# Optimization experiments

Measured on AMD Instinct MI355X. Metric: run time of the kernel, lower is better.

## Reference

```python
import jax, jax.numpy as jnp
import numpy as np

N_SRNA = 20000
N_MRNA = 100000
HID = 128
E_S2M = 1_000_000
E_M2M = 2_000_000
E_LBL = 500_000
N_LAYERS = 2


def setup_inputs() -> dict:
    key = jax.random.key(0)
    ks = jax.random.split(key, 20)
    s = 0.05
    inp = {
        # edge lists (rev edge types are flips, derived inside reference)
        "s2m_src": jax.random.randint(ks[0], (E_S2M,), 0, N_SRNA),
        "s2m_dst": jax.random.randint(ks[1], (E_S2M,), 0, N_MRNA),
        "m2m_src": jax.random.randint(ks[2], (E_M2M,), 0, N_MRNA),
        "m2m_dst": jax.random.randint(ks[3], (E_M2M,), 0, N_MRNA),
        "label_src": jax.random.randint(ks[4], (E_LBL,), 0, N_SRNA),
        "label_dst": jax.random.randint(ks[5], (E_LBL,), 0, N_MRNA),
        # embeddings (node_id is arange over all nodes -> identity lookup)
        "srna_emb": jax.random.normal(ks[6], (N_SRNA, HID), jnp.float32),
        "mrna_emb": jax.random.normal(ks[7], (N_MRNA, HID), jnp.float32),
        # per-layer stacked params. SAGEConv: out = lin_l(mean_agg)+lin_r(x_dst)
        "sage_s2m_Wl": jax.random.normal(ks[8], (N_LAYERS, HID, HID), jnp.float32) * s,
        "sage_s2m_bl": jnp.zeros((N_LAYERS, HID), jnp.float32),
        "sage_s2m_Wr": jax.random.normal(ks[9], (N_LAYERS, HID, HID), jnp.float32) * s,
        "sage_rev_Wl": jax.random.normal(ks[10], (N_LAYERS, HID, HID), jnp.float32) * s,
        "sage_rev_bl": jnp.zeros((N_LAYERS, HID), jnp.float32),
        "sage_rev_Wr": jax.random.normal(ks[11], (N_LAYERS, HID, HID), jnp.float32) * s,
        # GCNConv: out = propagate(norm, x @ W) + b
        "gcn_m2m_W": jax.random.normal(ks[12], (N_LAYERS, HID, HID), jnp.float32) * s,
        "gcn_m2m_b": jnp.zeros((N_LAYERS, HID), jnp.float32),
        "gcn_rev_W": jax.random.normal(ks[13], (N_LAYERS, HID, HID), jnp.float32) * s,
        "gcn_rev_b": jnp.zeros((N_LAYERS, HID), jnp.float32),
    }
    return inp


def _sage(x_src, x_dst, src, dst, n_dst, Wl, bl, Wr):
    # PyG SAGEConv (aggr='mean', root_weight=True): lin_l(mean_msg) + lin_r(x_dst)
    agg = jax.ops.segment_sum(x_src[src], dst, num_segments=n_dst)  # [n_dst, h]
    cnt = jax.ops.segment_sum(jnp.ones((src.shape[0],), x_src.dtype), dst,
                              num_segments=n_dst)
    agg = agg / jnp.maximum(cnt, 1.0)[:, None]
    return agg @ Wl + bl + x_dst @ Wr


def _gcn(x, src, dst, n, W, b):
    # PyG GCNConv: add self-loops, sym-normalize, x @ W, propagate, + bias
    xw = x @ W  # [n, h]
    deg = jax.ops.segment_sum(jnp.ones((src.shape[0],), x.dtype), dst,
                              num_segments=n) + 1.0  # +1 self-loop
    dinv = jax.lax.rsqrt(deg)
    norm = dinv[src] * dinv[dst]  # [E]
    out = jax.ops.segment_sum(norm[:, None] * xw[src], dst, num_segments=n)
    out = out + (dinv * dinv)[:, None] * xw  # self-loop term
    return out + b


def reference(s2m_src, s2m_dst, m2m_src, m2m_dst, label_src, label_dst,
              srna_emb, mrna_emb,
              sage_s2m_Wl, sage_s2m_bl, sage_s2m_Wr,
              sage_rev_Wl, sage_rev_bl, sage_rev_Wr,
              gcn_m2m_W, gcn_m2m_b, gcn_rev_W, gcn_rev_b):
    x_s, x_m = srna_emb, mrna_emb
    for l in range(N_LAYERS):
        # HeteroConv aggr='sum' over edge types per dst node type
        m_new = _sage(x_s, x_m, s2m_src, s2m_dst, N_MRNA,
                      sage_s2m_Wl[l], sage_s2m_bl[l], sage_s2m_Wr[l])
        m_new = m_new + _gcn(x_m, m2m_src, m2m_dst, N_MRNA,
                             gcn_m2m_W[l], gcn_m2m_b[l])
        m_new = m_new + _gcn(x_m, m2m_dst, m2m_src, N_MRNA,
                             gcn_rev_W[l], gcn_rev_b[l])  # rev_similar = flip
        s_new = _sage(x_m, x_s, s2m_dst, s2m_src, N_SRNA,
                      sage_rev_Wl[l], sage_rev_bl[l], sage_rev_Wr[l])
        x_s, x_m = jax.nn.relu(s_new), jax.nn.relu(m_new)
    # Classifier: dot product over labeled (srna, mrna) pairs
    return (x_s[label_src] * x_m[label_dst]).sum(axis=-1)
```

## Files before the change

### kernel.cpp

```cpp
#include <hip/hip_runtime.h>
#include <hip/hip_fp16.h>

#define NS 20000
#define NM 100000
#define H  128
#define ES 1000000
#define EM 2000000
#define EL 500000

#define SH_M 7
#define SH_S 6
#define NB_SD 782
#define NB_SS 313
#define NB_MD 782
#define NB_MS 782
#define CAP_SD 1664
#define CAP_SS 3904
#define CAP_MD 3200
#define CAP_MS 3200
#define MAXCAP 3904
#define CHUNK 4096
#define B_SD ((ES + CHUNK - 1) / CHUNK)
#define B_SS ((ES + CHUNK - 1) / CHUNK)
#define B_MD ((EM + CHUNK - 1) / CHUNK)
#define B_MS ((EM + CHUNK - 1) / CHUNK)
#define VAL_MASK 0x1FFFF

typedef _Float16 half8 __attribute__((ext_vector_type(8)));
typedef float floatx4 __attribute__((ext_vector_type(4)));

__global__ __launch_bounds__(256) void place1_sorted(
        const int* __restrict__ s2m_src, const int* __restrict__ s2m_dst,
        const int* __restrict__ m2m_src, const int* __restrict__ m2m_dst,
        int* __restrict__ bc,
        unsigned int* __restrict__ p_sd, unsigned int* __restrict__ p_ss,
        unsigned int* __restrict__ p_md, unsigned int* __restrict__ p_ms) {
    __shared__ unsigned int rec[CHUNK];
    __shared__ unsigned short eb[CHUNK];
    __shared__ int cnt[1024];
    __shared__ int gbase[1024];

    int b = blockIdx.x;
    const int *keys, *vals; int shift, cap, E, bcoff; unsigned int* pp;
    int cb;
    if (b < B_SD)                    { cb = b;                      keys = s2m_dst; vals = s2m_src; shift = SH_M; cap = CAP_SD; E = ES; bcoff = 0;     pp = p_sd; }
    else if (b < B_SD+B_SS)          { cb = b - B_SD;               keys = s2m_src; vals = s2m_dst; shift = SH_S; cap = CAP_SS; E = ES; bcoff = 16384; pp = p_ss; }
    else if (b < B_SD+B_SS+B_MD)     { cb = b - B_SD - B_SS;        keys = m2m_dst; vals = m2m_src; shift = SH_M; cap = CAP_MD; E = EM; bcoff = 32768; pp = p_md; }
    else                             { cb = b - B_SD - B_SS - B_MD; keys = m2m_src; vals = m2m_dst; shift = SH_M; cap = CAP_MS; E = EM; bcoff = 49152; pp = p_ms; }
    int* bcp = bc + bcoff;

    int t = threadIdx.x;
    int e0 = cb * CHUNK;
    int nv = E - e0; if (nv > CHUNK) nv = CHUNK;

    for (int i = t; i < nv; i += 256) {
        int k = keys[e0 + i];
        int v = vals[e0 + i];
        int bkt = k >> shift;
        rec[i] = ((unsigned int)(k - (bkt << shift)) << 17) | (unsigned int)v;
        eb[i] = (unsigned short)bkt;
    }
#pragma unroll
    for (int j = 0; j < 4; ++j) cnt[t * 4 + j] = 0;
    __syncthreads();
    for (int i = t; i < nv; i += 256) atomicAdd(&cnt[eb[i]], 1);
    __syncthreads();
#pragma unroll
    for (int j = 0; j < 4; ++j) {
        int bk = t * 4 + j;
        int c = cnt[bk];
        if (c > 0) {
            gbase[bk] = atomicAdd(&bcp[bk << 4], c);
            cnt[bk] = 0;
        }
    }
    __syncthreads();
    for (int i = t; i < nv; i += 256) {
        int bk = eb[i];
        int pos = atomicAdd(&cnt[bk], 1);
        int o = gbase[bk] + pos;
        if (o < cap) pp[(size_t)bk * cap + o] = rec[i];
    }
}

__global__ __launch_bounds__(1024) void bscan(const int* __restrict__ bc,
                                              int* __restrict__ bbase) {
    __shared__ int sh[1024];
    int c = blockIdx.x;
    int n = (c == 0) ? NB_SD : (c == 1) ? NB_SS : (c == 2) ? NB_MD : NB_MS;
    const int* bcp = bc + c * 16384;
    int t = threadIdx.x;
    int v = (t < n) ? bcp[t << 4] : 0;
    sh[t] = v;
    __syncthreads();
    for (int d = 1; d < 1024; d <<= 1) {
        int x = 0;
        if (t >= d) x = sh[t - d];
        __syncthreads();
        if (t >= d) sh[t] += x;
        __syncthreads();
    }
    if (t < n) bbase[c * 1024 + t] = sh[t] - v;
}

__global__ __launch_bounds__(256) void place2_fused(
        const int* __restrict__ bc, const int* __restrict__ bbase,
        const unsigned int* __restrict__ p_sd, const unsigned int* __restrict__ p_ss,
        const unsigned int* __restrict__ p_md, const unsigned int* __restrict__ p_ms,
        int* __restrict__ adj_sd, int* __restrict__ adj_ss,
        int* __restrict__ adj_md, int* __restrict__ adj_ms,
        int* __restrict__ off_sd, int* __restrict__ off_ss,
        int* __restrict__ off_md, int* __restrict__ off_ms,
        int* __restrict__ cnt_sd, int* __restrict__ cnt_ss,
        int* __restrict__ cnt_md, int* __restrict__ cnt_ms) {
    __shared__ unsigned int lp[MAXCAP];
    __shared__ int hist[128], cur[128], sbuf[128];
    int b = blockIdx.x;
    int c, lb;
    if (b < NB_SD)                    { c = 0; lb = b; }
    else if (b < NB_SD+NB_SS)         { c = 1; lb = b - NB_SD; }
    else if (b < NB_SD+NB_SS+NB_MD)   { c = 2; lb = b - NB_SD - NB_SS; }
    else                              { c = 3; lb = b - NB_SD - NB_SS - NB_MD; }
    const unsigned int* pp; int *adj, *offp, *cntp; int shift, cap, n;
    switch (c) {
    case 0:  pp = p_sd; adj = adj_sd; offp = off_sd; cntp = cnt_sd; shift = SH_M; cap = CAP_SD; n = NM; break;
    case 1:  pp = p_ss; adj = adj_ss; offp = off_ss; cntp = cnt_ss; shift = SH_S; cap = CAP_SS; n = NS; break;
    case 2:  pp = p_md; adj = adj_md; offp = off_md; cntp = cnt_md; shift = SH_M; cap = CAP_MD; n = NM; break;
    default: pp = p_ms; adj = adj_ms; offp = off_ms; cntp = cnt_ms; shift = SH_M; cap = CAP_MS; n = NM; break;
    }
    int t = threadIdx.x;
    int k = bc[c * 16384 + (lb << 4)];
    if (k > cap) k = cap;
    int base = lb << shift;
    int npb = 1 << shift;
    int bb = bbase[c * 1024 + lb];
    for (int i = t; i < k; i += 256) lp[i] = pp[(size_t)lb * cap + i];
    if (t < npb) hist[t] = 0;
    __syncthreads();
    for (int i = t; i < k; i += 256) atomicAdd(&hist[lp[i] >> 17], 1);
    __syncthreads();
    int v = (t < npb) ? hist[t] : 0;
    if (t < 128) sbuf[t] = v;
    __syncthreads();
    for (int d = 1; d < 128; d <<= 1) {
        int x = 0;
        if (t >= d && t < 128) x = sbuf[t - d];
        __syncthreads();
        if (t >= d && t < 128) sbuf[t] += x;
        __syncthreads();
    }
    if (t < npb) {
        int excl = sbuf[t] - v;
        cur[t] = excl;
        int node = base + t;
        if (node < n) { offp[node] = bb + excl; cntp[node] = v; }
    }
    __syncthreads();
    for (int i = t; i < k; i += 256) {
        unsigned int p = lp[i];
        int pos = atomicAdd(&cur[p >> 17], 1);
        adj[bb + pos] = (int)(p & VAL_MASK);
    }
}

__global__ void finalize_scales(const int* __restrict__ c_md, const int* __restrict__ c_ms,
                                float* __restrict__ dvf, float* __restrict__ dvr) {
    int i = blockIdx.x * blockDim.x + threadIdx.x;
    if (i < NM) {
        dvf[i] = rsqrtf((float)c_md[i] + 1.0f);
        dvr[i] = rsqrtf((float)c_ms[i] + 1.0f);
    }
}

__global__ void to_half(const float* __restrict__ in, __half* __restrict__ out,
                        long long n4) {
    long long i = (long long)blockIdx.x * blockDim.x + threadIdx.x;
    if (i >= n4) return;
    float4 v = *(const float4*)&in[i * 4];
    __half2 h0 = __floats2half2_rn(v.x, v.y);
    __half2 h1 = __floats2half2_rn(v.z, v.w);
    __half2* o = (__half2*)&out[i * 4];
    o[0] = h0; o[1] = h1;
}

__global__ void prep_w(const float* __restrict__ w0, const float* __restrict__ w1,
                       const float* __restrict__ w2, const float* __restrict__ w3,
                       const float* __restrict__ w4, const float* __restrict__ w5,
                       __half* __restrict__ out) {
    int idx = blockIdx.x * 256 + threadIdx.x;
    if (idx >= 12 * H * H) return;
    int mat = idx / (H * H);
    int rem = idx % (H * H);
    int n = rem / H;
    int k = rem % H;
    const float* base;
    switch (mat >> 1) {
    case 0: base = w0; break; case 1: base = w1; break; case 2: base = w2; break;
    case 3: base = w3; break; case 4: base = w4; break; default: base = w5; break;
    }
    base += (size_t)(mat & 1) * H * H;
    out[(size_t)mat * H * H + (size_t)n * H + k] = __float2half(base[(size_t)k * H + n]);
}

__device__ __forceinline__ float4 ldh4(const __half* __restrict__ X, long long idx) {
    float2 raw = *(const float2*)(X + idx);
    __half2 h0 = *(__half2*)&raw.x;
    __half2 h1 = *(__half2*)&raw.y;
    float2 fa = __half22float2(h0);
    float2 fb = __half22float2(h1);
    return make_float4(fa.x, fa.y, fb.x, fb.y);
}

__device__ __forceinline__ void sth4(__half* __restrict__ X, long long idx, float4 v) {
    float2 raw;
    *(__half2*)&raw.x = __floats2half2_rn(v.x, v.y);
    *(__half2*)&raw.y = __floats2half2_rn(v.z, v.w);
    *(float2*)(X + idx) = raw;
}

__device__ __forceinline__ float4 gather_plain(const __half* __restrict__ X,
                                               const int* __restrict__ adj,
                                               int o, int k, int c) {
    float4 acc = make_float4(0.f, 0.f, 0.f, 0.f);
    int j = 0;
    for (; j + 4 <= k; j += 4) {
        int s0 = adj[o + j], s1 = adj[o + j + 1], s2 = adj[o + j + 2], s3 = adj[o + j + 3];
        float4 v0 = ldh4(X, (long long)s0 * H + c);
        float4 v1 = ldh4(X, (long long)s1 * H + c);
        float4 v2 = ldh4(X, (long long)s2 * H + c);
        float4 v3 = ldh4(X, (long long)s3 * H + c);
        acc.x += v0.x + v1.x + v2.x + v3.x;
        acc.y += v0.y + v1.y + v2.y + v3.y;
        acc.z += v0.z + v1.z + v2.z + v3.z;
        acc.w += v0.w + v1.w + v2.w + v3.w;
    }
    for (; j < k; ++j) {
        int s = adj[o + j];
        float4 v = ldh4(X, (long long)s * H + c);
        acc.x += v.x; acc.y += v.y; acc.z += v.z; acc.w += v.w;
    }
    return acc;
}

__device__ __forceinline__ float4 gather_weighted(const __half* __restrict__ X,
                                                  const int* __restrict__ adj,
                                                  const float* __restrict__ dinv,
                                                  int o, int k, int c) {
    float4 acc = make_float4(0.f, 0.f, 0.f, 0.f);
    int j = 0;
    for (; j + 4 <= k; j += 4) {
        int s0 = adj[o + j], s1 = adj[o + j + 1], s2 = adj[o + j + 2], s3 = adj[o + j + 3];
        float d0 = dinv[s0], d1 = dinv[s1], d2 = dinv[s2], d3 = dinv[s3];
        float4 v0 = ldh4(X, (long long)s0 * H + c);
        float4 v1 = ldh4(X, (long long)s1 * H + c);
        float4 v2 = ldh4(X, (long long)s2 * H + c);
        float4 v3 = ldh4(X, (long long)s3 * H + c);
        acc.x += d0 * v0.x + d1 * v1.x + d2 * v2.x + d3 * v3.x;
        acc.y += d0 * v0.y + d1 * v1.y + d2 * v2.y + d3 * v3.y;
        acc.z += d0 * v0.z + d1 * v1.z + d2 * v2.z + d3 * v3.z;
        acc.w += d0 * v0.w + d1 * v1.w + d2 * v2.w + d3 * v3.w;
    }
    for (; j < k; ++j) {
        int s = adj[o + j];
        float ds = dinv[s];
        float4 v = ldh4(X, (long long)s * H + c);
        acc.x += ds * v.x; acc.y += ds * v.y; acc.z += ds * v.z; acc.w += ds * v.w;
    }
    return acc;
}

__global__ void mega_gather(const __half* __restrict__ xs16, const __half* __restrict__ xm16,
                            const int* __restrict__ off_sd, const int* __restrict__ cnt_sd,
                            const int* __restrict__ adj_sd,
                            const int* __restrict__ off_md, const int* __restrict__ cnt_md,
                            const int* __restrict__ adj_md,
                            const int* __restrict__ off_ms, const int* __restrict__ cnt_ms,
                            const int* __restrict__ adj_ms,
                            const int* __restrict__ off_ss, const int* __restrict__ cnt_ss,
                            const int* __restrict__ adj_ss,
                            const float* __restrict__ dvf, const float* __restrict__ dvr,
                            __half* __restrict__ SA, __half* __restrict__ Qf,
                            __half* __restrict__ Qr, __half* __restrict__ Qs) {
    long long gid = (long long)blockIdx.x * blockDim.x + threadIdx.x;
    int g = (int)(gid >> 5);
    int c = ((int)gid & 31) * 4;
    if (g < NM) {
        int k = cnt_sd[g];
        float4 acc = gather_plain(xs16, adj_sd, off_sd[g], k, c);
        float ic = 1.0f / fmaxf((float)k, 1.0f);
        acc.x *= ic; acc.y *= ic; acc.z *= ic; acc.w *= ic;
        sth4(SA, (long long)g * H + c, acc);
    } else if (g < 2 * NM) {
        int r = g - NM;
        float4 acc = gather_weighted(xm16, adj_md, dvf, off_md[r], cnt_md[r], c);
        float dd = dvf[r];
        float s2 = dd * dd;
        float4 self = ldh4(xm16, (long long)r * H + c);
        float4 q = make_float4(dd * acc.x + s2 * self.x, dd * acc.y + s2 * self.y,
                               dd * acc.z + s2 * self.z, dd * acc.w + s2 * self.w);
        sth4(Qf, (long long)r * H + c, q);
    } else if (g < 3 * NM) {
        int r = g - 2 * NM;
        float4 acc = gather_weighted(xm16, adj_ms, dvr, off_ms[r], cnt_ms[r], c);
        float dd = dvr[r];
        float s2 = dd * dd;
        float4 self = ldh4(xm16, (long long)r * H + c);
        float4 q = make_float4(dd * acc.x + s2 * self.x, dd * acc.y + s2 * self.y,
                               dd * acc.z + s2 * self.z, dd * acc.w + s2 * self.w);
        sth4(Qr, (long long)r * H + c, q);
    } else if (g < 3 * NM + NS) {
        int r = g - 3 * NM;
        int k = cnt_ss[r];
        float4 acc = gather_plain(xm16, adj_ss, off_ss[r], k, c);
        float ic = 1.0f / fmaxf((float)k, 1.0f);
        acc.x *= ic; acc.y *= ic; acc.z *= ic; acc.w *= ic;
        sth4(Qs, (long long)r * H + c, acc);
    }
}

__device__ __forceinline__ void mfma_stage(const __half* __restrict__ A,
                                           const __half* __restrict__ Wt,
                                           int gr, int M, int nlo, int quad,
                                           floatx4 (&acc)[8]) {
#pragma unroll
    for (int k0 = 0; k0 < 128; k0 += 32) {
        half8 a;
        if (gr < M) {
            a = *(const half8*)(A + (size_t)gr * H + k0 + quad * 8);
        } else {
            float4 z = make_float4(0.f, 0.f, 0.f, 0.f);
            a = *(half8*)&z;
        }
#pragma unroll
        for (int t = 0; t < 8; ++t) {
            half8 b = *(const half8*)(Wt + (size_t)(t * 16 + nlo) * H + k0 + quad * 8);
            acc[t] = __builtin_amdgcn_mfma_f32_16x16x32_f16(a, b, acc[t], 0, 0, 0);
        }
    }
}

__global__ __launch_bounds__(256) void mega_gemm_mfma(
        const __half* __restrict__ SA, const __half* __restrict__ Qf,
        const __half* __restrict__ Qr, const __half* __restrict__ xm_in,
        const __half* __restrict__ Qs, const __half* __restrict__ xs_in,
        const __half* __restrict__ wbuf,
        const float* __restrict__ bl, const float* __restrict__ gb,
        const float* __restrict__ grb, const float* __restrict__ bls,
        __half* __restrict__ xm_out, __half* __restrict__ xs_out,
        int MBLK, int layer)
{
    const int tid = threadIdx.x;
    const int w = tid >> 6;
    const int lane = tid & 63;
    const int quad = lane >> 4;
    const int nlo = lane & 15;
    const size_t HH = (size_t)H * H;

    floatx4 acc[8];
#pragma unroll
    for (int t = 0; t < 8; ++t) {
        acc[t][0] = 0.f; acc[t][1] = 0.f; acc[t][2] = 0.f; acc[t][3] = 0.f;
    }

    if ((int)blockIdx.x < MBLK) {
        const int bm = blockIdx.x * 64 + w * 16;
        const int gr = bm + nlo;
        mfma_stage(SA,    wbuf + (0 * 2 + layer) * HH, gr, NM, nlo, quad, acc);
        mfma_stage(xm_in, wbuf + (1 * 2 + layer) * HH, gr, NM, nlo, quad, acc);
        mfma_stage(Qf,    wbuf + (2 * 2 + layer) * HH, gr, NM, nlo, quad, acc);
        mfma_stage(Qr,    wbuf + (3 * 2 + layer) * HH, gr, NM, nlo, quad, acc);
#pragma unroll
        for (int t = 0; t < 8; ++t) {
            int col = t * 16 + nlo;
            float bias = bl[col] + gb[col] + grb[col];
#pragma unroll
            for (int i = 0; i < 4; ++i) {
                int r = bm + quad * 4 + i;
                if (r < NM)
                    xm_out[(size_t)r * H + col] = __float2half(fmaxf(acc[t][i] + bias, 0.f));
            }
        }
    } else {
        const int bm = ((int)blockIdx.x - MBLK) * 64 + w * 16;
        const int gr = bm + nlo;
        mfma_stage(Qs,    wbuf + (4 * 2 + layer) * HH, gr, NS, nlo, quad, acc);
        mfma_stage(xs_in, wbuf + (5 * 2 + layer) * HH, gr, NS, nlo, quad, acc);
#pragma unroll
        for (int t = 0; t < 8; ++t) {
            int col = t * 16 + nlo;
            float bias = bls[col];
#pragma unroll
            for (int i = 0; i < 4; ++i) {
                int r = bm + quad * 4 + i;
                if (r < NS)
                    xs_out[(size_t)r * H + col] = __float2half(fmaxf(acc[t][i] + bias, 0.f));
            }
        }
    }
}

__global__ void classify(const __half* __restrict__ xs16, const __half* __restrict__ xm16,
                         const int* __restrict__ ls, const int* __restrict__ ld,
                         float* __restrict__ out, int P) {
    long long gid = (long long)blockIdx.x * blockDim.x + threadIdx.x;
    int p = (int)(gid >> 5);
    if (p >= P) return;
    int lane = (int)gid & 31;
    int a = ls[p], b = ld[p];
    float4 u = ldh4(xs16, (long long)a * H + lane * 4);
    float4 v = ldh4(xm16, (long long)b * H + lane * 4);
    float s = u.x * v.x + u.y * v.y + u.z * v.z + u.w * v.w;
    for (int off = 16; off > 0; off >>= 1) s += __shfl_down(s, off, 32);
    if (lane == 0) out[p] = s;
}

extern "C" void kernel_launch(void* const* d_in, const int* in_sizes, int n_in,
                              void* d_out, int out_size, void* d_ws, size_t ws_size,
                              hipStream_t stream) {
    const int* s2m_src = (const int*)d_in[0];
    const int* s2m_dst = (const int*)d_in[1];
    const int* m2m_src = (const int*)d_in[2];
    const int* m2m_dst = (const int*)d_in[3];
    const int* lbl_src = (const int*)d_in[4];
    const int* lbl_dst = (const int*)d_in[5];
    const float* s_emb = (const float*)d_in[6];
    const float* m_emb = (const float*)d_in[7];
    const float* Wl_s2m = (const float*)d_in[8];
    const float* bl_s2m = (const float*)d_in[9];
    const float* Wr_s2m = (const float*)d_in[10];
    const float* Wl_rev = (const float*)d_in[11];
    const float* bl_rev = (const float*)d_in[12];
    const float* Wr_rev = (const float*)d_in[13];
    const float* gW  = (const float*)d_in[14];
    const float* gb  = (const float*)d_in[15];
    const float* grW = (const float*)d_in[16];
    const float* grb = (const float*)d_in[17];

    __half* hws = (__half*)d_ws;
    size_t ho = 0;
    __half* xm16_a = hws + ho; ho += (size_t)NM * H;
    __half* xm16_b = hws + ho; ho += (size_t)NM * H;
    __half* xs16_a = hws + ho; ho += (size_t)NS * H;
    __half* xs16_b = hws + ho; ho += (size_t)NS * H;
    __half* SA = hws + ho; ho += (size_t)NM * H;
    __half* Qf = hws + ho; ho += (size_t)NM * H;
    __half* Qr = hws + ho; ho += (size_t)NM * H;
    __half* Qs = hws + ho; ho += (size_t)NS * H;
    __half* wbuf = hws + ho; ho += (size_t)12 * H * H;

    float* fws = (float*)(hws + ho);
    size_t fo = 0;
    float* dvf = fws + fo; fo += NM;
    float* dvr = fws + fo; fo += NM;

    int* ip = (int*)(fws + fo);
    size_t io = 0;
    int* off_sd = ip + io; io += NM;
    int* off_ss = ip + io; io += NS;
    int* off_md = ip + io; io += NM;
    int* off_ms = ip + io; io += NM;
    int* cnt_sd = ip + io; io += NM;
    int* cnt_ss = ip + io; io += NS;
    int* cnt_md = ip + io; io += NM;
    int* cnt_ms = ip + io; io += NM;
    int* bc     = ip + io; io += 4 * 16384;
    int* bbase  = ip + io; io += 4 * 1024;
    int* adj_sd = ip + io; io += ES;
    int* adj_ss = ip + io; io += ES;
    int* adj_md = ip + io; io += EM;
    int* adj_ms = ip + io; io += EM;

    unsigned int* p_sd = (unsigned int*)SA;
    unsigned int* p_ss = p_sd + (size_t)NB_SD * CAP_SD;
    unsigned int* p_md = p_ss + (size_t)NB_SS * CAP_SS;
    unsigned int* p_ms = p_md + (size_t)NB_MD * CAP_MD;

    const int bM = (NM + 255) / 256;

    hipMemsetAsync(bc, 0, 4 * 16384 * sizeof(int), stream);
    place1_sorted<<<B_SD + B_SS + B_MD + B_MS, 256, 0, stream>>>(
        s2m_src, s2m_dst, m2m_src, m2m_dst, bc, p_sd, p_ss, p_md, p_ms);
    bscan<<<4, 1024, 0, stream>>>(bc, bbase);
    place2_fused<<<NB_SD + NB_SS + NB_MD + NB_MS, 256, 0, stream>>>(
        bc, bbase, p_sd, p_ss, p_md, p_ms,
        adj_sd, adj_ss, adj_md, adj_ms,
        off_sd, off_ss, off_md, off_ms,
        cnt_sd, cnt_ss, cnt_md, cnt_ms);
    finalize_scales<<<bM, 256, 0, stream>>>(cnt_md, cnt_ms, dvf, dvr);

    const long long n4m = (long long)NM * H / 4;
    const long long n4s = (long long)NS * H / 4;
    to_half<<<(int)((n4m + 255) / 256), 256, 0, stream>>>(m_emb, xm16_a, n4m);
    to_half<<<(int)((n4s + 255) / 256), 256, 0, stream>>>(s_emb, xs16_a, n4s);
    prep_w<<<(12 * H * H + 255) / 256, 256, 0, stream>>>(
        Wl_s2m, Wr_s2m, gW, grW, Wl_rev, Wr_rev, wbuf);

    const int gMega = (int)(((long long)(3 * NM + NS) * 32 + 255) / 256);
    const int MBLK = (NM + 63) / 64;
    const int SBLK = (NS + 63) / 64;

    const __half* xin_m = xm16_a;
    const __half* xin_s = xs16_a;
    __half* xout_m = xm16_b;
    __half* xout_s = xs16_b;

    for (int l = 0; l < 2; ++l) {
        const size_t bo = (size_t)l * H;

        mega_gather<<<gMega, 256, 0, stream>>>(xin_s, xin_m,
                                               off_sd, cnt_sd, adj_sd,
                                               off_md, cnt_md, adj_md,
                                               off_ms, cnt_ms, adj_ms,
                                               off_ss, cnt_ss, adj_ss,
                                               dvf, dvr, SA, Qf, Qr, Qs);

        mega_gemm_mfma<<<MBLK + SBLK, 256, 0, stream>>>(
            SA, Qf, Qr, xin_m, Qs, xin_s, wbuf,
            bl_s2m + bo, gb + bo, grb + bo, bl_rev + bo,
            xout_m, xout_s, MBLK, l);

        const __half* tm = xin_m; xin_m = xout_m; xout_m = (__half*)tm;
        const __half* ts = xin_s; xin_s = xout_s; xout_s = (__half*)ts;
    }

    classify<<<(int)(((long long)EL * 32 + 255) / 256), 256, 0, stream>>>(
        xin_s, xin_m, lbl_src, lbl_dst, (float*)d_out, EL);
}
```

Measured before the change: 976.2 us.

## Widen gather to 8 halves per lane and drop bucket scan kernel

The gather now has each lane load 8 fp16 values (16 bytes) instead of 4, so a 128-wide row is covered by 16 lanes rather than 32, and it unrolls the neighbour loop to 8 to keep more loads in flight. The separate bucket prefix-scan kernel is removed. Adjacency lists are now laid out at fixed per-bucket capacity offsets, with padding between buckets, which saves a launch and a dependency. In exchange the adjacency buffers grow to capacity size, and each lane uses more registers.

```diff
diff --git a/kernel.cpp b/kernel.cpp
--- a/kernel.cpp
+++ b/kernel.cpp
@@ -83,28 +83,8 @@
     }
 }
 
-__global__ __launch_bounds__(1024) void bscan(const int* __restrict__ bc,
-                                              int* __restrict__ bbase) {
-    __shared__ int sh[1024];
-    int c = blockIdx.x;
-    int n = (c == 0) ? NB_SD : (c == 1) ? NB_SS : (c == 2) ? NB_MD : NB_MS;
-    const int* bcp = bc + c * 16384;
-    int t = threadIdx.x;
-    int v = (t < n) ? bcp[t << 4] : 0;
-    sh[t] = v;
-    __syncthreads();
-    for (int d = 1; d < 1024; d <<= 1) {
-        int x = 0;
-        if (t >= d) x = sh[t - d];
-        __syncthreads();
-        if (t >= d) sh[t] += x;
-        __syncthreads();
-    }
-    if (t < n) bbase[c * 1024 + t] = sh[t] - v;
-}
-
 __global__ __launch_bounds__(256) void place2_fused(
-        const int* __restrict__ bc, const int* __restrict__ bbase,
+        const int* __restrict__ bc,
         const unsigned int* __restrict__ p_sd, const unsigned int* __restrict__ p_ss,
         const unsigned int* __restrict__ p_md, const unsigned int* __restrict__ p_ms,
         int* __restrict__ adj_sd, int* __restrict__ adj_ss,
@@ -133,7 +113,7 @@
     if (k > cap) k = cap;
     int base = lb << shift;
     int npb = 1 << shift;
-    int bb = bbase[c * 1024 + lb];
+    int bb = lb * cap;
     for (int i = t; i < k; i += 256) lp[i] = pp[(size_t)lb * cap + i];
     if (t < npb) hist[t] = 0;
     __syncthreads();
@@ -159,7 +139,7 @@
     for (int i = t; i < k; i += 256) {
         unsigned int p = lp[i];
         int pos = atomicAdd(&cur[p >> 17], 1);
-        adj[bb + pos] = (int)(p & VAL_MASK);
+        adj[(size_t)bb + pos] = (int)(p & VAL_MASK);
     }
 }
 
@@ -211,62 +191,92 @@
     return make_float4(fa.x, fa.y, fb.x, fb.y);
 }
 
-__device__ __forceinline__ void sth4(__half* __restrict__ X, long long idx, float4 v) {
-    float2 raw;
-    *(__half2*)&raw.x = __floats2half2_rn(v.x, v.y);
-    *(__half2*)&raw.y = __floats2half2_rn(v.z, v.w);
-    *(float2*)(X + idx) = raw;
-}
-
-__device__ __forceinline__ float4 gather_plain(const __half* __restrict__ X,
-                                               const int* __restrict__ adj,
-                                               int o, int k, int c) {
-    float4 acc = make_float4(0.f, 0.f, 0.f, 0.f);
+__device__ __forceinline__ void gacc_plain(const __half* __restrict__ X,
+                                           const int* __restrict__ adj,
+                                           int o, int k, int c, float (&acc)[8]) {
     int j = 0;
+    for (; j + 8 <= k; j += 8) {
+        int s0 = adj[o+j+0], s1 = adj[o+j+1], s2 = adj[o+j+2], s3 = adj[o+j+3];
+        int s4 = adj[o+j+4], s5 = adj[o+j+5], s6 = adj[o+j+6], s7 = adj[o+j+7];
+        half8 v0 = *(const half8*)(X + (size_t)s0 * H + c);
+        half8 v1 = *(const half8*)(X + (size_t)s1 * H + c);
+        half8 v2 = *(const half8*)(X + (size_t)s2 * H + c);
+        half8 v3 = *(const half8*)(X + (size_t)s3 * H + c);
+        half8 v4 = *(const half8*)(X + (size_t)s4 * H + c);
+        half8 v5 = *(const half8*)(X + (size_t)s5 * H + c);
+        half8 v6 = *(const half8*)(X + (size_t)s6 * H + c);
+        half8 v7 = *(const half8*)(X + (size_t)s7 * H + c);
+#pragma unroll
+        for (int i = 0; i < 8; ++i)
+            acc[i] += (float)v0[i] + (float)v1[i] + (float)v2[i] + (float)v3[i]
+                    + (float)v4[i] + (float)v5[i] + (float)v6[i] + (float)v7[i];
+    }
     for (; j + 4 <= k; j += 4) {
-        int s0 = adj[o + j], s1 = adj[o + j + 1], s2 = adj[o + j + 2], s3 = adj[o + j + 3];
-        float4 v0 = ldh4(X, (long long)s0 * H + c);
-        float4 v1 = ldh4(X, (long long)s1 * H + c);
-        float4 v2 = ldh4(X, (long long)s2 * H + c);
-        float4 v3 = ldh4(X, (long long)s3 * H + c);
-        acc.x += v0.x + v1.x + v2.x + v3.x;
-        acc.y += v0.y + v1.y + v2.y + v3.y;
-        acc.z += v0.z + v1.z + v2.z + v3.z;
-        acc.w += v0.w + v1.w + v2.w + v3.w;
+        int s0 = adj[o+j+0], s1 = adj[o+j+1], s2 = adj[o+j+2], s3 = adj[o+j+3];
+        half8 v0 = *(const half8*)(X + (size_t)s0 * H + c);
+        half8 v1 = *(const half8*)(X + (size_t)s1 * H + c);
+        half8 v2 = *(const half8*)(X + (size_t)s2 * H + c);
+        half8 v3 = *(const half8*)(X + (size_t)s3 * H + c);
+#pragma unroll
+        for (int i = 0; i < 8; ++i)
+            acc[i] += (float)v0[i] + (float)v1[i] + (float)v2[i] + (float)v3[i];
     }
     for (; j < k; ++j) {
         int s = adj[o + j];
-        float4 v = ldh4(X, (long long)s * H + c);
-        acc.x += v.x; acc.y += v.y; acc.z += v.z; acc.w += v.w;
-    }
-    return acc;
-}
-
-__device__ __forceinline__ float4 gather_weighted(const __half* __restrict__ X,
-                                                  const int* __restrict__ adj,
-                                                  const float* __restrict__ dinv,
-                                                  int o, int k, int c) {
-    float4 acc = make_float4(0.f, 0.f, 0.f, 0.f);
+        half8 v = *(const half8*)(X + (size_t)s * H + c);
+#pragma unroll
+        for (int i = 0; i < 8; ++i) acc[i] += (float)v[i];
+    }
+}
+
+__device__ __forceinline__ void gacc_weighted(const __half* __restrict__ X,
+                                              const int* __restrict__ adj,
+                                              const float* __restrict__ dinv,
+                                              int o, int k, int c, float (&acc)[8]) {
     int j = 0;
+    for (; j + 8 <= k; j += 8) {
+        int s0 = adj[o+j+0], s1 = adj[o+j+1], s2 = adj[o+j+2], s3 = adj[o+j+3];
+        int s4 = adj[o+j+4], s5 = adj[o+j+5], s6 = adj[o+j+6], s7 = adj[o+j+7];
+        float d0 = dinv[s0], d1 = dinv[s1], d2 = dinv[s2], d3 = dinv[s3];
+        float d4 = dinv[s4], d5 = dinv[s5], d6 = dinv[s6], d7 = dinv[s7];
+        half8 v0 = *(const half8*)(X + (size_t)s0 * H + c);
+        half8 v1 = *(const half8*)(X + (size_t)s1 * H + c);
+        half8 v2 = *(const half8*)(X + (size_t)s2 * H + c);
+        half8 v3 = *(const half8*)(X + (size_t)s3 * H + c);
+        half8 v4 = *(const half8*)(X + (size_t)s4 * H + c);
+        half8 v5 = *(const half8*)(X + (size_t)s5 * H + c);
+        half8 v6 = *(const half8*)(X + (size_t)s6 * H + c);
+        half8 v7 = *(const half8*)(X + (size_t)s7 * H + c);
+#pragma unroll
+        for (int i = 0; i < 8; ++i)
+            acc[i] += d0 * (float)v0[i] + d1 * (float)v1[i] + d2 * (float)v2[i] + d3 * (float)v3[i]
+                    + d4 * (float)v4[i] + d5 * (float)v5[i] + d6 * (float)v6[i] + d7 * (float)v7[i];
+    }
     for (; j + 4 <= k; j += 4) {
-        int s0 = adj[o + j], s1 = adj[o + j + 1], s2 = adj[o + j + 2], s3 = adj[o + j + 3];
+        int s0 = adj[o+j+0], s1 = adj[o+j+1], s2 = adj[o+j+2], s3 = adj[o+j+3];
         float d0 = dinv[s0], d1 = dinv[s1], d2 = dinv[s2], d3 = dinv[s3];
-        float4 v0 = ldh4(X, (long long)s0 * H + c);
-        float4 v1 = ldh4(X, (long long)s1 * H + c);
-        float4 v2 = ldh4(X, (long long)s2 * H + c);
-        float4 v3 = ldh4(X, (long long)s3 * H + c);
-        acc.x += d0 * v0.x + d1 * v1.x + d2 * v2.x + d3 * v3.x;
-        acc.y += d0 * v0.y + d1 * v1.y + d2 * v2.y + d3 * v3.y;
-        acc.z += d0 * v0.z + d1 * v1.z + d2 * v2.z + d3 * v3.z;
-        acc.w += d0 * v0.w + d1 * v1.w + d2 * v2.w + d3 * v3.w;
+        half8 v0 = *(const half8*)(X + (size_t)s0 * H + c);
+        half8 v1 = *(const half8*)(X + (size_t)s1 * H + c);
+        half8 v2 = *(const half8*)(X + (size_t)s2 * H + c);
+        half8 v3 = *(const half8*)(X + (size_t)s3 * H + c);
+#pragma unroll
+        for (int i = 0; i < 8; ++i)
+            acc[i] += d0 * (float)v0[i] + d1 * (float)v1[i] + d2 * (float)v2[i] + d3 * (float)v3[i];
     }
     for (; j < k; ++j) {
         int s = adj[o + j];
         float ds = dinv[s];
-        float4 v = ldh4(X, (long long)s * H + c);
-        acc.x += ds * v.x; acc.y += ds * v.y; acc.z += ds * v.z; acc.w += ds * v.w;
-    }
-    return acc;
+        half8 v = *(const half8*)(X + (size_t)s * H + c);
+#pragma unroll
+        for (int i = 0; i < 8; ++i) acc[i] += ds * (float)v[i];
+    }
+}
+
+__device__ __forceinline__ void sth8(__half* __restrict__ X, size_t idx, const float (&a)[8]) {
+    half8 h;
+#pragma unroll
+    for (int i = 0; i < 8; ++i) h[i] = (_Float16)a[i];
+    *(half8*)(X + idx) = h;
 }
 
 __global__ void mega_gather(const __half* __restrict__ xs16, const __half* __restrict__ xm16,
@@ -282,39 +292,42 @@
                             __half* __restrict__ SA, __half* __restrict__ Qf,
                             __half* __restrict__ Qr, __half* __restrict__ Qs) {
     long long gid = (long long)blockIdx.x * blockDim.x + threadIdx.x;
-    int g = (int)(gid >> 5);
-    int c = ((int)gid & 31) * 4;
+    int g = (int)(gid >> 4);
+    int c = ((int)gid & 15) * 8;
+    float acc[8] = {0.f, 0.f, 0.f, 0.f, 0.f, 0.f, 0.f, 0.f};
     if (g < NM) {
         int k = cnt_sd[g];
-        float4 acc = gather_plain(xs16, adj_sd, off_sd[g], k, c);
+        gacc_plain(xs16, adj_sd, off_sd[g], k, c, acc);
         float ic = 1.0f / fmaxf((float)k, 1.0f);
-        acc.x *= ic; acc.y *= ic; acc.z *= ic; acc.w *= ic;
-        sth4(SA, (long long)g * H + c, acc);
+#pragma unroll
+        for (int i = 0; i < 8; ++i) acc[i] *= ic;
+        sth8(SA, (size_t)g * H + c, acc);
     } else if (g < 2 * NM) {
         int r = g - NM;
-        float4 acc = gather_weighted(xm16, adj_md, dvf, off_md[r], cnt_md[r], c);
+        gacc_weighted(xm16, adj_md, dvf, off_md[r], cnt_md[r], c, acc);
         float dd = dvf[r];
         float s2 = dd * dd;
-        float4 self = ldh4(xm16, (long long)r * H + c);
-        float4 q = make_float4(dd * acc.x + s2 * self.x, dd * acc.y + s2 * self.y,
-                               dd * acc.z + s2 * self.z, dd * acc.w + s2 * self.w);
-        sth4(Qf, (long long)r * H + c, q);
+        half8 self = *(const half8*)(xm16 + (size_t)r * H + c);
+#pragma unroll
+        for (int i = 0; i < 8; ++i) acc[i] = dd * acc[i] + s2 * (float)self[i];
+        sth8(Qf, (size_t)r * H + c, acc);
     } else if (g < 3 * NM) {
         int r = g - 2 * NM;
-        float4 acc = gather_weighted(xm16, adj_ms, dvr, off_ms[r], cnt_ms[r], c);
+        gacc_weighted(xm16, adj_ms, dvr, off_ms[r], cnt_ms[r], c, acc);
         float dd = dvr[r];
         float s2 = dd * dd;
-        float4 self = ldh4(xm16, (long long)r * H + c);
-        float4 q = make_float4(dd * acc.x + s2 * self.x, dd * acc.y + s2 * self.y,
-                               dd * acc.z + s2 * self.z, dd * acc.w + s2 * self.w);
-        sth4(Qr, (long long)r * H + c, q);
+        half8 self = *(const half8*)(xm16 + (size_t)r * H + c);
+#pragma unroll
+        for (int i = 0; i < 8; ++i) acc[i] = dd * acc[i] + s2 * (float)self[i];
+        sth8(Qr, (size_t)r * H + c, acc);
     } else if (g < 3 * NM + NS) {
         int r = g - 3 * NM;
         int k = cnt_ss[r];
-        float4 acc = gather_plain(xm16, adj_ss, off_ss[r], k, c);
+        gacc_plain(xm16, adj_ss, off_ss[r], k, c, acc);
         float ic = 1.0f / fmaxf((float)k, 1.0f);
-        acc.x *= ic; acc.y *= ic; acc.z *= ic; acc.w *= ic;
-        sth4(Qs, (long long)r * H + c, acc);
+#pragma unroll
+        for (int i = 0; i < 8; ++i) acc[i] *= ic;
+        sth8(Qs, (size_t)r * H + c, acc);
     }
 }
 
@@ -464,11 +477,10 @@
     int* cnt_md = ip + io; io += NM;
     int* cnt_ms = ip + io; io += NM;
     int* bc     = ip + io; io += 4 * 16384;
-    int* bbase  = ip + io; io += 4 * 1024;
-    int* adj_sd = ip + io; io += ES;
-    int* adj_ss = ip + io; io += ES;
-    int* adj_md = ip + io; io += EM;
-    int* adj_ms = ip + io; io += EM;
+    int* adj_sd = ip + io; io += NB_SD * CAP_SD;
+    int* adj_ss = ip + io; io += NB_SS * CAP_SS;
+    int* adj_md = ip + io; io += NB_MD * CAP_MD;
+    int* adj_ms = ip + io; io += NB_MS * CAP_MS;
 
     unsigned int* p_sd = (unsigned int*)SA;
     unsigned int* p_ss = p_sd + (size_t)NB_SD * CAP_SD;
@@ -480,9 +492,8 @@
     hipMemsetAsync(bc, 0, 4 * 16384 * sizeof(int), stream);
     place1_sorted<<<B_SD + B_SS + B_MD + B_MS, 256, 0, stream>>>(
         s2m_src, s2m_dst, m2m_src, m2m_dst, bc, p_sd, p_ss, p_md, p_ms);
-    bscan<<<4, 1024, 0, stream>>>(bc, bbase);
     place2_fused<<<NB_SD + NB_SS + NB_MD + NB_MS, 256, 0, stream>>>(
-        bc, bbase, p_sd, p_ss, p_md, p_ms,
+        bc, p_sd, p_ss, p_md, p_ms,
         adj_sd, adj_ss, adj_md, adj_ms,
         off_sd, off_ss, off_md, off_ms,
         cnt_sd, cnt_ss, cnt_md, cnt_ms);
@@ -495,7 +506,7 @@
     prep_w<<<(12 * H * H + 255) / 256, 256, 0, stream>>>(
         Wl_s2m, Wr_s2m, gW, grW, Wl_rev, Wr_rev, wbuf);
 
-    const int gMega = (int)(((long long)(3 * NM + NS) * 32 + 255) / 256);
+    const int gMega = (int)(((long long)(3 * NM + NS) * 16 + 255) / 256);
     const int MBLK = (NM + 63) / 64;
     const int SBLK = (NS + 63) / 64;
 
```

After: 967.5 us. About the same (-0.9%).
